# Kernel optimization log

Hardware: AMD Instinct MI355X
Metric: run time of the kernel (lower is better)

## Reference

```python
import jax, jax.numpy as jnp
import numpy as np

THRESHOLD = 0.5
N_SEG = 5
NEG_INF = -1e30
EPS = 1e-12  # F.normalize eps


def setup_inputs() -> dict:
    key = jax.random.key(0)
    kx, kl = jax.random.split(key)
    B, D, L = 4096, 512, 80
    x = jax.random.normal(kx, (B, D), dtype=jnp.float32)
    labels = jax.random.randint(kl, (B, L), 0, 2, dtype=jnp.int32)
    return {"x": x, "labels": labels}


def reference(x, labels):
    B = x.shape[0]
    labels_f = labels.astype(jnp.float32)
    # pairwise Jaccard over multi-hot labels
    intersection = labels_f @ labels_f.T                      # [B, B]
    counts = labels_f.sum(axis=1, keepdims=True)              # [B, 1]
    union = counts + counts.T - intersection
    jaccard = intersection / union                            # [B, B]
    # cosine similarity (F.normalize with eps clamp)
    norm = jnp.maximum(jnp.linalg.norm(x, axis=1, keepdims=True), EPS)
    nx = x / norm
    sim = nx @ nx.T                                           # [B, B]
    # --- sample positive (uniform among jaccard > threshold), fixed key ---
    pos_mask = jaccard > THRESHOLD
    valid_mask = jnp.any(pos_mask, axis=1)                    # [B]
    logits = jnp.where(pos_mask, 0.0, NEG_INF)
    sampled = jax.random.categorical(jax.random.key(42), logits, axis=-1)
    pos_samples = jnp.where(valid_mask, sampled, 0)           # invalid rows -> 0
    # --- top-k negatives: jaccard strictly below the positive's jaccard ---
    pos_sim_j = jaccard[jnp.arange(B), pos_samples]           # [B]
    neg_mask = jaccard < pos_sim_j[:, None]
    neg_sims = jnp.where(neg_mask, jaccard, -jnp.inf)
    _, neg_samples = jax.lax.top_k(neg_sims, N_SEG)           # [B, N_SEG]
    # --- contrastive loss on cosine sims at sampled indices ---
    rel_pos = sim[jnp.arange(B), pos_samples]                 # [B]
    rel_neg = jnp.take_along_axis(sim, neg_samples, axis=1)   # [B, N_SEG]
    exp_pos = jnp.exp(rel_pos)
    sum_exp_neg = jnp.exp(rel_neg).sum(axis=1)
    loss = -jnp.log(exp_pos / (exp_pos + sum_exp_neg))
    vm = valid_mask.astype(x.dtype)
    return (loss * vm).sum() / vm.sum()
```

## Files before the change

kernel.cpp:

```cpp
#include <hip/hip_runtime.h>
#include <stdint.h>

#define B_ROWS 4096
#define DIMS   512
#define NLAB   80
#define HALF_ROWS 2048
#define HCNT   8388608u
#define CHUNK  1024
#define SEGCAP 256u

typedef unsigned long long u64;

__device__ __forceinline__ uint32_t rotl32(uint32_t x, uint32_t d) {
    return (x << d) | (x >> (32u - d));
}

__device__ __forceinline__ void tf2x32_key42(uint32_t c0, uint32_t c1,
                                             uint32_t& o0, uint32_t& o1) {
    const uint32_t ks0 = 0u;
    const uint32_t ks1 = 42u;
    const uint32_t ks2 = 0x1BD11BDAu ^ 0u ^ 42u;
    uint32_t x0 = c0 + ks0;
    uint32_t x1 = c1 + ks1;
#define TF_RND(r) { x0 += x1; x1 = rotl32(x1, (r)); x1 ^= x0; }
    TF_RND(13u) TF_RND(15u) TF_RND(26u) TF_RND(6u)
    x0 += ks1; x1 += ks2 + 1u;
    TF_RND(17u) TF_RND(29u) TF_RND(16u) TF_RND(24u)
    x0 += ks2; x1 += ks0 + 2u;
    TF_RND(13u) TF_RND(15u) TF_RND(26u) TF_RND(6u)
    x0 += ks0; x1 += ks1 + 3u;
    TF_RND(17u) TF_RND(29u) TF_RND(16u) TF_RND(24u)
    x0 += ks1; x1 += ks2 + 4u;
    TF_RND(13u) TF_RND(15u) TF_RND(26u) TF_RND(6u)
    x0 += ks2; x1 += ks0 + 5u;
#undef TF_RND
    o0 = x0; o1 = x1;
}

__device__ __forceinline__ u64 shflx64(u64 v, int m) {
    uint32_t lo = __shfl_xor((uint32_t)(v & 0xFFFFFFFFull), m, 64);
    uint32_t hi = __shfl_xor((uint32_t)(v >> 32), m, 64);
    return ((u64)hi << 32) | (u64)lo;
}

__device__ __forceinline__ uint32_t umx(uint32_t a, uint32_t b) { return a > b ? a : b; }
__device__ __forceinline__ uint32_t umn(uint32_t a, uint32_t b) { return a < b ? a : b; }

__device__ __forceinline__ void ins5_u32(uint32_t* t, uint32_t k) {
    t[4] = umx(t[4], k);
    uint32_t hi, lo;
    hi = umx(t[3], t[4]); lo = umn(t[3], t[4]); t[3] = hi; t[4] = lo;
    hi = umx(t[2], t[3]); lo = umn(t[2], t[3]); t[2] = hi; t[3] = lo;
    hi = umx(t[1], t[2]); lo = umn(t[1], t[2]); t[1] = hi; t[2] = lo;
    hi = umx(t[0], t[1]); lo = umn(t[0], t[1]); t[0] = hi; t[1] = lo;
}

__device__ __forceinline__ void merge5_u32(uint32_t* A, const uint32_t* Bv) {
    uint32_t a0=A[0],a1=A[1],a2=A[2],a3=A[3],a4=A[4];
    uint32_t b0=Bv[0],b1=Bv[1],b2=Bv[2],b3=Bv[3],b4=Bv[4];
    uint32_t m0 = umx(a0, b0);
    uint32_t m1 = umx(umx(a1, b1), umn(a0, b0));
    uint32_t m2 = umx(umx(a2, b2), umx(umn(a0, b1), umn(a1, b0)));
    uint32_t m3 = umx(umx(a3, b3), umx(umx(umn(a0, b2), umn(a1, b1)), umn(a2, b0)));
    uint32_t m4 = umx(umx(a4, b4), umx(umx(umn(a0, b3), umn(a1, b2)),
                                       umx(umn(a2, b1), umn(a3, b0))));
    A[0]=m0; A[1]=m1; A[2]=m2; A[3]=m3; A[4]=m4;
}

__device__ __forceinline__ uint32_t jkey19(uint32_t it, uint32_t u) {
    const uint32_t n = it << 19;
    float f = (float)it * __builtin_amdgcn_rcpf((float)u) * 524288.0f;
    uint32_t ak = (uint32_t)f;
    int r = (int)(n - ak * u);
    if (r < 0) { ak--; r += (int)u; }
    if (r >= (int)u) ak++;
    return ak + 1u;
}


__global__ __launch_bounds__(256) void prep_kernel(const float* __restrict__ x,
                                                   const int* __restrict__ labels,
                                                   uint4* __restrict__ pk,
                                                   float* __restrict__ norms) {
    const int tid = threadIdx.x;
    const int lane = tid & 63;
    const int row = blockIdx.x * 4 + (tid >> 6);
    const int* lr = labels + (size_t)row * NLAB;
    const int la = lr[lane];
    const int lb = (lane < 16) ? lr[64 + lane] : 0;
    const u64 b0 = __ballot(la != 0);
    const u64 b1 = __ballot(lb != 0);
    const uint32_t w2 = (uint32_t)b1 & 0xFFFFu;
    const uint32_t cnt = (uint32_t)__popcll(b0) + (uint32_t)__popc(w2);
    if (lane == 0) pk[row] = make_uint4((uint32_t)b0, (uint32_t)(b0 >> 32), w2, cnt);
    const float* xr = x + (size_t)row * DIMS;
    float ss = 0.f;
#pragma unroll
    for (int u = 0; u < 8; ++u) { float v = xr[lane + 64 * u]; ss += v * v; }
#pragma unroll
    for (int m = 1; m < 64; m <<= 1) ss += __shfl_xor(ss, m, 64);
    if (lane == 0) norms[row] = fmaxf(sqrtf(ss), 1e-12f);
}

__global__ __launch_bounds__(256) void scan_kernel(const uint4* __restrict__ pk,
                                                   uint32_t* __restrict__ scnt,
                                                   uint32_t* __restrict__ sList,
                                                   uint32_t* __restrict__ keys5P) {
    __shared__ uint4 tab[CHUNK];
    const int tid = threadIdx.x;
    const int grp = (int)blockIdx.x >> 2;
    const int sub = (int)blockIdx.x & 3;
    const int jbase = sub * CHUNK;
#pragma unroll
    for (int k = 0; k < 4; ++k) tab[tid + 256 * k] = pk[jbase + tid + 256 * k];

    const int lane = tid & 63;
    const int pr = grp * 4 + (tid >> 6);
    const int r0 = pr, r1 = pr + HALF_ROWS;
    const uint4 P0 = pk[r0], P1 = pk[r1];
    const uint32_t cw0 = P0.w, cw1 = P1.w;
    uint32_t* seg0 = sList + ((((uint32_t)r0 << 2) | sub) << 8);
    uint32_t* seg1 = sList + ((((uint32_t)r1 << 2) | sub) << 8);
    uint32_t cnt0 = 0u, cnt1 = 0u;

    uint32_t t0[5], t1[5];
#pragma unroll
    for (int k = 0; k < 5; ++k) {
        const uint32_t fk = (uint32_t)(~(jbase + k)) & 0xFFFu;
        t0[k] = fk; t1[k] = fk;
    }
    __syncthreads();

#pragma unroll 4
    for (int jb = 0; jb < CHUNK; jb += 64) {
        const int jl = jb + lane;
        const int j  = jbase + jl;
        const uint4 pj = tab[jl];
        const uint32_t cj = pj.w;
        const uint32_t jx = (~(uint32_t)j) & 0xFFFu;
        const uint32_t it0 = (uint32_t)(__popc(P0.x & pj.x) + __popc(P0.y & pj.y) + __popc(P0.z & pj.z));
        const uint32_t u0  = cw0 + cj - it0;
        const uint32_t it1 = (uint32_t)(__popc(P1.x & pj.x) + __popc(P1.y & pj.y) + __popc(P1.z & pj.z));
        const uint32_t u1  = cw1 + cj - it1;
        const bool c0 = (it0 << 1) > u0;
        const bool c1 = (it1 << 1) > u1;
        const u64 bal0 = __ballot(c0);
        const u64 bal1 = __ballot(c1);
        if (bal0) {
            if (c0) {
                const uint32_t off = cnt0 + (uint32_t)__popcll(bal0 & ((1ull << lane) - 1ull));
                if (off < SEGCAP) seg0[off] = (it0 << 20) | (u0 << 12) | (uint32_t)j;
            }
            cnt0 += (uint32_t)__popcll(bal0);
        } else {
            const uint32_t thr = umx(t0[4] >> 12, 1u) - 1u;
            if ((it0 << 19) >= __umul24(thr, u0))
                ins5_u32(t0, (jkey19(it0, u0) << 12) | jx);
        }
        if (!c0 && bal0) {
            const uint32_t thr = umx(t0[4] >> 12, 1u) - 1u;
            if ((it0 << 19) >= __umul24(thr, u0))
                ins5_u32(t0, (jkey19(it0, u0) << 12) | jx);
        }
        if (bal1) {
            if (c1) {
                const uint32_t off = cnt1 + (uint32_t)__popcll(bal1 & ((1ull << lane) - 1ull));
                if (off < SEGCAP) seg1[off] = (it1 << 20) | (u1 << 12) | (uint32_t)j;
            }
            cnt1 += (uint32_t)__popcll(bal1);
        } else {
            const uint32_t thr = umx(t1[4] >> 12, 1u) - 1u;
            if ((it1 << 19) >= __umul24(thr, u1))
                ins5_u32(t1, (jkey19(it1, u1) << 12) | jx);
        }
        if (!c1 && bal1) {
            const uint32_t thr = umx(t1[4] >> 12, 1u) - 1u;
            if ((it1 << 19) >= __umul24(thr, u1))
                ins5_u32(t1, (jkey19(it1, u1) << 12) | jx);
        }
    }
#pragma unroll
    for (int m = 1; m < 64; m <<= 1) {
        uint32_t o[5];
#pragma unroll
        for (int k = 0; k < 5; ++k) o[k] = __shfl_xor(t0[k], m, 64);
        merge5_u32(t0, o);
#pragma unroll
        for (int k = 0; k < 5; ++k) o[k] = __shfl_xor(t1[k], m, 64);
        merge5_u32(t1, o);
    }
    if (lane == 0) {
        scnt[((uint32_t)r0 << 2) | sub] = cnt0;
        scnt[((uint32_t)r1 << 2) | sub] = cnt1;
        const int idx = (pr << 2) | sub;
#pragma unroll
        for (int k = 0; k < 5; ++k) {
            keys5P[idx * 10 + k]     = t0[k];
            keys5P[idx * 10 + 5 + k] = t1[k];
        }
    }
}

__global__ __launch_bounds__(256) void fin_kernel(const float* __restrict__ x,
                                                  const float* __restrict__ norms,
                                                  const uint32_t* __restrict__ scnt,
                                                  const uint32_t* __restrict__ sList,
                                                  const uint32_t* __restrict__ keys5P,
                                                  float2* __restrict__ blockPart) {
    __shared__ float lossW[4], cntW[4];
    const int tid = threadIdx.x;
    const int lane = tid & 63;
    const int w = tid >> 6;
    const int row = (int)blockIdx.x * 4 + w;
    const int pr   = row & (HALF_ROWS - 1);
    const int half = row >> 11;
    const uint32_t rbase = (uint32_t)row << 2;

    const float* xr = x + (size_t)row * DIMS;
    float v[8];
#pragma unroll
    for (int u = 0; u < 8; ++u) v[u] = xr[lane + 64 * u];
    uint32_t ns[4];
#pragma unroll
    for (int s = 0; s < 4; ++s) ns[s] = umn(scnt[rbase + s], SEGCAP);

    uint32_t f[5];
#pragma unroll
    for (int k = 0; k < 5; ++k) f[k] = keys5P[((pr << 2) | 0) * 10 + half * 5 + k];
#pragma unroll
    for (int s = 1; s < 4; ++s) {
        uint32_t o[5];
#pragma unroll
        for (int k = 0; k < 5; ++k) o[k] = keys5P[((pr << 2) | s) * 10 + half * 5 + k];
        merge5_u32(f, o);
    }

    const uint32_t base23 = (uint32_t)pr * (uint32_t)B_ROWS;
    u64 gb = 0ull;
    for (int s = 0; s < 4; ++s) {
        const uint32_t* sl = sList + ((rbase + s) << 8);
        for (int e = lane; e < (int)ns[s]; e += 64) {
            const uint32_t ent = sl[e];
            const uint32_t j  = ent & 0xFFFu;
            const uint32_t u  = (ent >> 12) & 0xFFu;
            const uint32_t it = ent >> 20;
            uint32_t o0, o1;
            tf2x32_key42(base23 + j, base23 + j + HCNT, o0, o1);
            const uint32_t o = half ? o1 : o0;
            const u64 key = ((u64)(o >> 9) << 41) | ((u64)((~j) & 0xFFFu) << 29) | (u64)jkey19(it, u);
            if (key > gb) gb = key;
        }
    }
#pragma unroll
    for (int m = 1; m < 64; m <<= 1) {
        const u64 o = shflx64(gb, m);
        if (o > gb) gb = o;
    }
    const bool valid = gb != 0ull;
    const int pos = valid ? (int)((~(uint32_t)(gb >> 29)) & 0xFFFu) : 0;
    const uint32_t pjkey = (uint32_t)(gb & 0xFFFFFu);

    uint32_t ts[5] = {0u, 0u, 0u, 0u, 0u};
    for (int s = 0; s < 4; ++s) {
        const uint32_t* sl = sList + ((rbase + s) << 8);
        for (int e = lane; e < (int)ns[s]; e += 64) {
            const uint32_t ent = sl[e];
            const uint32_t j  = ent & 0xFFFu;
            const uint32_t u  = (ent >> 12) & 0xFFu;
            const uint32_t it = ent >> 20;
            const uint32_t k19 = jkey19(it, u);
            if (k19 < pjkey) ins5_u32(ts, (k19 << 12) | ((~j) & 0xFFFu));
        }
    }
#pragma unroll
    for (int m = 1; m < 64; m <<= 1) {
        uint32_t o[5];
#pragma unroll
        for (int k = 0; k < 5; ++k) o[k] = __shfl_xor(ts[k], m, 64);
        merge5_u32(ts, o);
    }
    merge5_u32(f, ts);

    int tg[6];
    tg[0] = pos;
#pragma unroll
    for (int k = 0; k < 5; ++k) tg[k + 1] = (int)((~f[k]) & 0xFFFu);

    const float* pp[6];
#pragma unroll
    for (int q = 0; q < 6; ++q) pp[q] = x + (size_t)tg[q] * DIMS;
    float dot[6] = {0.f,0.f,0.f,0.f,0.f,0.f};
#pragma unroll
    for (int u = 0; u < 8; ++u) {
#pragma unroll
        for (int q = 0; q < 6; ++q) dot[q] += v[u] * pp[q][lane + 64 * u];
    }
#pragma unroll
    for (int m = 1; m < 64; m <<= 1) {
#pragma unroll
        for (int q = 0; q < 6; ++q) dot[q] += __shfl_xor(dot[q], m, 64);
    }

    if (lane == 0) {
        float loss = 0.f, cnt = 0.f;
        if (valid) {
            const float nr = norms[row];
            const float sp = dot[0] / (nr * norms[tg[0]]);
            float sen = 0.f;
#pragma unroll
            for (int q = 1; q < 6; ++q) sen += expf(dot[q] / (nr * norms[tg[q]]));
            const float ep = expf(sp);
            loss = -logf(ep / (ep + sen));
            cnt = 1.f;
        }
        lossW[w] = loss; cntW[w] = cnt;
    }
    __syncthreads();
    if (tid == 0) {
        blockPart[blockIdx.x] = make_float2(lossW[0] + lossW[1] + lossW[2] + lossW[3],
                                            cntW[0] + cntW[1] + cntW[2] + cntW[3]);
    }
}

__global__ __launch_bounds__(256) void final_kernel(const float2* __restrict__ blockPart,
                                                    float* __restrict__ out) {
    __shared__ float rl[4], rc[4];
    const int tid = threadIdx.x;
    const int lane = tid & 63;
    const int w = tid >> 6;
    float sl = 0.f, sc = 0.f;
#pragma unroll
    for (int k = 0; k < 4; ++k) {
        const float2 p = blockPart[tid + 256 * k];
        sl += p.x; sc += p.y;
    }
#pragma unroll
    for (int m = 1; m < 64; m <<= 1) {
        sl += __shfl_xor(sl, m, 64);
        sc += __shfl_xor(sc, m, 64);
    }
    if (lane == 0) { rl[w] = sl; rc[w] = sc; }
    __syncthreads();
    if (tid == 0) out[0] = (rl[0] + rl[1] + rl[2] + rl[3]) / (rc[0] + rc[1] + rc[2] + rc[3]);
}

extern "C" void kernel_launch(void* const* d_in, const int* in_sizes, int n_in,
                              void* d_out, int out_size, void* d_ws, size_t ws_size,
                              hipStream_t stream) {
    const float* x      = (const float*)d_in[0];
    const int*   labels = (const int*)d_in[1];
    float* out = (float*)d_out;

    char* ws = (char*)d_ws;
    uint4*    pk     = (uint4*)ws;
    float*    norms  = (float*)(ws + 65536);
    uint32_t* scnt   = (uint32_t*)(ws + 65536 + 16384);
    uint32_t* keys5P = (uint32_t*)(ws + 65536 + 16384 + 65536);
    float2*   bPart  = (float2*)(ws + 65536 + 16384 + 65536 + 327680);
    uint32_t* sList  = (uint32_t*)(ws + (1u << 20));

    hipLaunchKernelGGL(prep_kernel,  dim3(1024), dim3(256), 0, stream, x, labels, pk, norms);
    hipLaunchKernelGGL(scan_kernel,  dim3(2048), dim3(256), 0, stream, pk, scnt, sList, keys5P);
    hipLaunchKernelGGL(fin_kernel,   dim3(1024), dim3(256), 0, stream, x, norms, scnt, sList, keys5P, bPart);
    hipLaunchKernelGGL(final_kernel, dim3(1),    dim3(256), 0, stream, bPart, out);
}
```

Measured before the change: 101.4 us.

## Fuse scan and finalize kernels with per-row-pair blocks and LDS segment lists

Merges the candidate scan and finalize kernels into one kernel where each block handles one row pair, and each of its four waves scans a quarter of the columns. Positive-candidate lists, counts and partial top-5 keys stay in shared memory instead of going through global workspace, which removes one launch and the global round trip. The scan loop is simplified to a single branch per row, with the insertion threshold cached in a register, and the six dot products are spread across waves. In exchange, column data is now read straight from global/L2 instead of an LDS table, and some waves sit idle during the finalize phase.

```diff
diff --git a/kernel.cpp b/kernel.cpp
--- a/kernel.cpp
+++ b/kernel.cpp
@@ -102,40 +102,41 @@
     if (lane == 0) norms[row] = fmaxf(sqrtf(ss), 1e-12f);
 }
 
-__global__ __launch_bounds__(256) void scan_kernel(const uint4* __restrict__ pk,
-                                                   uint32_t* __restrict__ scnt,
-                                                   uint32_t* __restrict__ sList,
-                                                   uint32_t* __restrict__ keys5P) {
-    __shared__ uint4 tab[CHUNK];
+__global__ __launch_bounds__(256) void fused_kernel(const float* __restrict__ x,
+                                                    const uint4* __restrict__ pk,
+                                                    const float* __restrict__ norms,
+                                                    float2* __restrict__ blockPart) {
+    __shared__ uint32_t segL[2][4][SEGCAP];
+    __shared__ uint32_t cntL[2][4];
+    __shared__ uint32_t keysL[2][4][5];
+    __shared__ uint32_t tgL[2][6];
+    __shared__ uint32_t validL[2];
+    __shared__ float    simsL[2][6];
+    __shared__ float    lossW[2], cntW2[2];
+
     const int tid = threadIdx.x;
-    const int grp = (int)blockIdx.x >> 2;
-    const int sub = (int)blockIdx.x & 3;
-    const int jbase = sub * CHUNK;
-#pragma unroll
-    for (int k = 0; k < 4; ++k) tab[tid + 256 * k] = pk[jbase + tid + 256 * k];
-
     const int lane = tid & 63;
-    const int pr = grp * 4 + (tid >> 6);
+    const int sub  = tid >> 6;
+    const int pr   = (int)blockIdx.x;
     const int r0 = pr, r1 = pr + HALF_ROWS;
     const uint4 P0 = pk[r0], P1 = pk[r1];
     const uint32_t cw0 = P0.w, cw1 = P1.w;
-    uint32_t* seg0 = sList + ((((uint32_t)r0 << 2) | sub) << 8);
-    uint32_t* seg1 = sList + ((((uint32_t)r1 << 2) | sub) << 8);
+    const int jbase = sub * CHUNK;
+
     uint32_t cnt0 = 0u, cnt1 = 0u;
-
     uint32_t t0[5], t1[5];
 #pragma unroll
     for (int k = 0; k < 5; ++k) {
         const uint32_t fk = (uint32_t)(~(jbase + k)) & 0xFFFu;
         t0[k] = fk; t1[k] = fk;
     }
-    __syncthreads();
+    uint32_t thr0 = umx(t0[4] >> 12, 1u) - 1u;
+    uint32_t thr1 = umx(t1[4] >> 12, 1u) - 1u;
 
 #pragma unroll 4
     for (int jb = 0; jb < CHUNK; jb += 64) {
-        const int jl = jb + lane;
-        const int j  = jbase + jl;
-        const uint4 pj = tab[jl];
+        const int j = jbase + jb + lane;
+        const uint4 pj = pk[j];
         const uint32_t cj = pj.w;
         const uint32_t jx = (~(uint32_t)j) & 0xFFFu;
         const uint32_t it0 = (uint32_t)(__popc(P0.x & pj.x) + __popc(P0.y & pj.y) + __popc(P0.z & pj.z));
@@ -146,38 +147,23 @@
         const bool c1 = (it1 << 1) > u1;
         const u64 bal0 = __ballot(c0);
         const u64 bal1 = __ballot(c1);
-        if (bal0) {
-            if (c0) {
-                const uint32_t off = cnt0 + (uint32_t)__popcll(bal0 & ((1ull << lane) - 1ull));
-                if (off < SEGCAP) seg0[off] = (it0 << 20) | (u0 << 12) | (uint32_t)j;
-            }
-            cnt0 += (uint32_t)__popcll(bal0);
-        } else {
-            const uint32_t thr = umx(t0[4] >> 12, 1u) - 1u;
-            if ((it0 << 19) >= __umul24(thr, u0))
-                ins5_u32(t0, (jkey19(it0, u0) << 12) | jx);
-        }
-        if (!c0 && bal0) {
-            const uint32_t thr = umx(t0[4] >> 12, 1u) - 1u;
-            if ((it0 << 19) >= __umul24(thr, u0))
-                ins5_u32(t0, (jkey19(it0, u0) << 12) | jx);
-        }
-        if (bal1) {
-            if (c1) {
-                const uint32_t off = cnt1 + (uint32_t)__popcll(bal1 & ((1ull << lane) - 1ull));
-                if (off < SEGCAP) seg1[off] = (it1 << 20) | (u1 << 12) | (uint32_t)j;
-            }
-            cnt1 += (uint32_t)__popcll(bal1);
-        } else {
-            const uint32_t thr = umx(t1[4] >> 12, 1u) - 1u;
-            if ((it1 << 19) >= __umul24(thr, u1))
-                ins5_u32(t1, (jkey19(it1, u1) << 12) | jx);
-        }
-        if (!c1 && bal1) {
-            const uint32_t thr = umx(t1[4] >> 12, 1u) - 1u;
-            if ((it1 << 19) >= __umul24(thr, u1))
-                ins5_u32(t1, (jkey19(it1, u1) << 12) | jx);
-        }
+        const u64 lmask = (1ull << lane) - 1ull;
+        if (c0) {
+            const uint32_t off = cnt0 + (uint32_t)__popcll(bal0 & lmask);
+            if (off < SEGCAP) segL[0][sub][off] = (it0 << 20) | (u0 << 12) | (uint32_t)j;
+        } else if ((it0 << 19) >= __umul24(thr0, u0)) {
+            ins5_u32(t0, (jkey19(it0, u0) << 12) | jx);
+            thr0 = umx(t0[4] >> 12, 1u) - 1u;
+        }
+        cnt0 += (uint32_t)__popcll(bal0);
+        if (c1) {
+            const uint32_t off = cnt1 + (uint32_t)__popcll(bal1 & lmask);
+            if (off < SEGCAP) segL[1][sub][off] = (it1 << 20) | (u1 << 12) | (uint32_t)j;
+        } else if ((it1 << 19) >= __umul24(thr1, u1)) {
+            ins5_u32(t1, (jkey19(it1, u1) << 12) | jx);
+            thr1 = umx(t1[4] >> 12, 1u) - 1u;
+        }
+        cnt1 += (uint32_t)__popcll(bal1);
     }
 #pragma unroll
     for (int m = 1; m < 64; m <<= 1) {
@@ -190,136 +176,119 @@
         merge5_u32(t1, o);
     }
     if (lane == 0) {
-        scnt[((uint32_t)r0 << 2) | sub] = cnt0;
-        scnt[((uint32_t)r1 << 2) | sub] = cnt1;
-        const int idx = (pr << 2) | sub;
-#pragma unroll
-        for (int k = 0; k < 5; ++k) {
-            keys5P[idx * 10 + k]     = t0[k];
-            keys5P[idx * 10 + 5 + k] = t1[k];
-        }
-    }
-}
-
-__global__ __launch_bounds__(256) void fin_kernel(const float* __restrict__ x,
-                                                  const float* __restrict__ norms,
-                                                  const uint32_t* __restrict__ scnt,
-                                                  const uint32_t* __restrict__ sList,
-                                                  const uint32_t* __restrict__ keys5P,
-                                                  float2* __restrict__ blockPart) {
-    __shared__ float lossW[4], cntW[4];
-    const int tid = threadIdx.x;
-    const int lane = tid & 63;
-    const int w = tid >> 6;
-    const int row = (int)blockIdx.x * 4 + w;
-    const int pr   = row & (HALF_ROWS - 1);
-    const int half = row >> 11;
-    const uint32_t rbase = (uint32_t)row << 2;
-
-    const float* xr = x + (size_t)row * DIMS;
-    float v[8];
-#pragma unroll
-    for (int u = 0; u < 8; ++u) v[u] = xr[lane + 64 * u];
-    uint32_t ns[4];
-#pragma unroll
-    for (int s = 0; s < 4; ++s) ns[s] = umn(scnt[rbase + s], SEGCAP);
-
-    uint32_t f[5];
-#pragma unroll
-    for (int k = 0; k < 5; ++k) f[k] = keys5P[((pr << 2) | 0) * 10 + half * 5 + k];
-#pragma unroll
-    for (int s = 1; s < 4; ++s) {
-        uint32_t o[5];
-#pragma unroll
-        for (int k = 0; k < 5; ++k) o[k] = keys5P[((pr << 2) | s) * 10 + half * 5 + k];
-        merge5_u32(f, o);
-    }
-
-    const uint32_t base23 = (uint32_t)pr * (uint32_t)B_ROWS;
-    u64 gb = 0ull;
-    for (int s = 0; s < 4; ++s) {
-        const uint32_t* sl = sList + ((rbase + s) << 8);
-        for (int e = lane; e < (int)ns[s]; e += 64) {
-            const uint32_t ent = sl[e];
-            const uint32_t j  = ent & 0xFFFu;
-            const uint32_t u  = (ent >> 12) & 0xFFu;
-            const uint32_t it = ent >> 20;
-            uint32_t o0, o1;
-            tf2x32_key42(base23 + j, base23 + j + HCNT, o0, o1);
-            const uint32_t o = half ? o1 : o0;
-            const u64 key = ((u64)(o >> 9) << 41) | ((u64)((~j) & 0xFFFu) << 29) | (u64)jkey19(it, u);
-            if (key > gb) gb = key;
-        }
-    }
-#pragma unroll
-    for (int m = 1; m < 64; m <<= 1) {
-        const u64 o = shflx64(gb, m);
-        if (o > gb) gb = o;
-    }
-    const bool valid = gb != 0ull;
-    const int pos = valid ? (int)((~(uint32_t)(gb >> 29)) & 0xFFFu) : 0;
-    const uint32_t pjkey = (uint32_t)(gb & 0xFFFFFu);
-
-    uint32_t ts[5] = {0u, 0u, 0u, 0u, 0u};
-    for (int s = 0; s < 4; ++s) {
-        const uint32_t* sl = sList + ((rbase + s) << 8);
-        for (int e = lane; e < (int)ns[s]; e += 64) {
-            const uint32_t ent = sl[e];
-            const uint32_t j  = ent & 0xFFFu;
-            const uint32_t u  = (ent >> 12) & 0xFFu;
-            const uint32_t it = ent >> 20;
-            const uint32_t k19 = jkey19(it, u);
-            if (k19 < pjkey) ins5_u32(ts, (k19 << 12) | ((~j) & 0xFFFu));
-        }
-    }
-#pragma unroll
-    for (int m = 1; m < 64; m <<= 1) {
-        uint32_t o[5];
-#pragma unroll
-        for (int k = 0; k < 5; ++k) o[k] = __shfl_xor(ts[k], m, 64);
-        merge5_u32(ts, o);
-    }
-    merge5_u32(f, ts);
-
-    int tg[6];
-    tg[0] = pos;
-#pragma unroll
-    for (int k = 0; k < 5; ++k) tg[k + 1] = (int)((~f[k]) & 0xFFFu);
-
-    const float* pp[6];
-#pragma unroll
-    for (int q = 0; q < 6; ++q) pp[q] = x + (size_t)tg[q] * DIMS;
-    float dot[6] = {0.f,0.f,0.f,0.f,0.f,0.f};
-#pragma unroll
-    for (int u = 0; u < 8; ++u) {
-#pragma unroll
-        for (int q = 0; q < 6; ++q) dot[q] += v[u] * pp[q][lane + 64 * u];
-    }
-#pragma unroll
-    for (int m = 1; m < 64; m <<= 1) {
-#pragma unroll
-        for (int q = 0; q < 6; ++q) dot[q] += __shfl_xor(dot[q], m, 64);
-    }
-
-    if (lane == 0) {
+        cntL[0][sub] = cnt0; cntL[1][sub] = cnt1;
+#pragma unroll
+        for (int k = 0; k < 5; ++k) { keysL[0][sub][k] = t0[k]; keysL[1][sub][k] = t1[k]; }
+    }
+    __syncthreads();
+
+    if (sub < 2) {
+        const int h = sub;
+        uint32_t f[5];
+#pragma unroll
+        for (int k = 0; k < 5; ++k) f[k] = keysL[h][0][k];
+#pragma unroll
+        for (int s = 1; s < 4; ++s) {
+            uint32_t o[5];
+#pragma unroll
+            for (int k = 0; k < 5; ++k) o[k] = keysL[h][s][k];
+            merge5_u32(f, o);
+        }
+        uint32_t ns[4];
+#pragma unroll
+        for (int s = 0; s < 4; ++s) ns[s] = umn(cntL[h][s], SEGCAP);
+
+        const uint32_t base23 = (uint32_t)pr * (uint32_t)B_ROWS;
+        u64 gb = 0ull;
+#pragma unroll
+        for (int s = 0; s < 4; ++s) {
+            for (int e = lane; e < (int)ns[s]; e += 64) {
+                const uint32_t ent = segL[h][s][e];
+                const uint32_t j  = ent & 0xFFFu;
+                const uint32_t u  = (ent >> 12) & 0xFFu;
+                const uint32_t it = ent >> 20;
+                uint32_t o0, o1;
+                tf2x32_key42(base23 + j, base23 + j + HCNT, o0, o1);
+                const uint32_t o = h ? o1 : o0;
+                const u64 key = ((u64)(o >> 9) << 41) | ((u64)((~j) & 0xFFFu) << 29) | (u64)jkey19(it, u);
+                if (key > gb) gb = key;
+            }
+        }
+#pragma unroll
+        for (int m = 1; m < 64; m <<= 1) {
+            const u64 o = shflx64(gb, m);
+            if (o > gb) gb = o;
+        }
+        const bool valid = gb != 0ull;
+        const int pos = valid ? (int)((~(uint32_t)(gb >> 29)) & 0xFFFu) : 0;
+        const uint32_t pjkey = (uint32_t)(gb & 0xFFFFFu);
+
+        uint32_t ts[5] = {0u, 0u, 0u, 0u, 0u};
+#pragma unroll
+        for (int s = 0; s < 4; ++s) {
+            for (int e = lane; e < (int)ns[s]; e += 64) {
+                const uint32_t ent = segL[h][s][e];
+                const uint32_t j  = ent & 0xFFFu;
+                const uint32_t u  = (ent >> 12) & 0xFFu;
+                const uint32_t it = ent >> 20;
+                const uint32_t k19 = jkey19(it, u);
+                if (k19 < pjkey) ins5_u32(ts, (k19 << 12) | ((~j) & 0xFFFu));
+            }
+        }
+#pragma unroll
+        for (int m = 1; m < 64; m <<= 1) {
+            uint32_t o[5];
+#pragma unroll
+            for (int k = 0; k < 5; ++k) o[k] = __shfl_xor(ts[k], m, 64);
+            merge5_u32(ts, o);
+        }
+        merge5_u32(f, ts);
+
+        if (lane == 0) {
+            tgL[h][0] = (uint32_t)pos;
+#pragma unroll
+            for (int k = 0; k < 5; ++k) tgL[h][k + 1] = (~f[k]) & 0xFFFu;
+            validL[h] = valid ? 1u : 0u;
+        }
+    }
+    __syncthreads();
+
+#pragma unroll
+    for (int k = 0; k < 3; ++k) {
+        const int d = sub + 4 * k;
+        const int h = (d >= 6) ? 1 : 0;
+        const int q = d - 6 * h;
+        const int row = h ? r1 : r0;
+        const int tgt = (int)tgL[h][q];
+        const float* pa = x + (size_t)row * DIMS;
+        const float* pb = x + (size_t)tgt * DIMS;
+        float s = 0.f;
+#pragma unroll
+        for (int u = 0; u < 8; ++u) s += pa[lane + 64 * u] * pb[lane + 64 * u];
+#pragma unroll
+        for (int m = 1; m < 64; m <<= 1) s += __shfl_xor(s, m, 64);
+        if (lane == 0) simsL[h][q] = s;
+    }
+    __syncthreads();
+
+    if (sub < 2 && lane == 0) {
+        const int h = sub;
         float loss = 0.f, cnt = 0.f;
-        if (valid) {
+        if (validL[h]) {
+            const int row = h ? r1 : r0;
             const float nr = norms[row];
-            const float sp = dot[0] / (nr * norms[tg[0]]);
+            const float sp = simsL[h][0] / (nr * norms[tgL[h][0]]);
             float sen = 0.f;
 #pragma unroll
-            for (int q = 1; q < 6; ++q) sen += expf(dot[q] / (nr * norms[tg[q]]));
+            for (int q = 1; q < 6; ++q) sen += expf(simsL[h][q] / (nr * norms[tgL[h][q]]));
             const float ep = expf(sp);
             loss = -logf(ep / (ep + sen));
             cnt = 1.f;
         }
-        lossW[w] = loss; cntW[w] = cnt;
-    }
-    __syncthreads();
-    if (tid == 0) {
-        blockPart[blockIdx.x] = make_float2(lossW[0] + lossW[1] + lossW[2] + lossW[3],
-                                            cntW[0] + cntW[1] + cntW[2] + cntW[3]);
-    }
+        lossW[h] = loss; cntW2[h] = cnt;
+    }
+    __syncthreads();
+    if (tid == 0) blockPart[pr] = make_float2(lossW[0] + lossW[1], cntW2[0] + cntW2[1]);
 }
 
 __global__ __launch_bounds__(256) void final_kernel(const float2* __restrict__ blockPart,
@@ -330,7 +299,7 @@
     const int w = tid >> 6;
     float sl = 0.f, sc = 0.f;
 #pragma unroll
-    for (int k = 0; k < 4; ++k) {
+    for (int k = 0; k < 8; ++k) {
         const float2 p = blockPart[tid + 256 * k];
         sl += p.x; sc += p.y;
     }
@@ -352,15 +321,11 @@
     float* out = (float*)d_out;
 
     char* ws = (char*)d_ws;
-    uint4*    pk     = (uint4*)ws;
-    float*    norms  = (float*)(ws + 65536);
-    uint32_t* scnt   = (uint32_t*)(ws + 65536 + 16384);
-    uint32_t* keys5P = (uint32_t*)(ws + 65536 + 16384 + 65536);
-    float2*   bPart  = (float2*)(ws + 65536 + 16384 + 65536 + 327680);
-    uint32_t* sList  = (uint32_t*)(ws + (1u << 20));
+    uint4*  pk    = (uint4*)ws;
+    float*  norms = (float*)(ws + 65536);
+    float2* bPart = (float2*)(ws + 65536 + 16384);
 
     hipLaunchKernelGGL(prep_kernel,  dim3(1024), dim3(256), 0, stream, x, labels, pk, norms);
-    hipLaunchKernelGGL(scan_kernel,  dim3(2048), dim3(256), 0, stream, pk, scnt, sList, keys5P);
-    hipLaunchKernelGGL(fin_kernel,   dim3(1024), dim3(256), 0, stream, x, norms, scnt, sList, keys5P, bPart);
+    hipLaunchKernelGGL(fused_kernel, dim3(2048), dim3(256), 0, stream, x, pk, norms, bPart);
     hipLaunchKernelGGL(final_kernel, dim3(1),    dim3(256), 0, stream, bPart, out);
 }
```

Measured after the change: 100.9 us. About the same (-0.5%).
